# Performance work log

Hardware: AMD Instinct MI355X
Metric: run time of the kernel (lower is better)

## Reference

```python
import jax, jax.numpy as jnp
import numpy as np

N = 262144
E = N * 32
C_W = 7.0 / np.pi  # Wendland C2 2D normalization


def kernel_gradient(q, dirs, h):
    # torchSPHv2 wendland gradient: -dir * C/h^3 * 20 q (1-q)^3, q = r/h in [0,1]
    mag = (C_W / h ** 3) * 20.0 * q * (1.0 - q) ** 3
    return -dirs * mag[:, None]


def setup_inputs() -> dict:
    key = jax.random.key(0)
    ks = jax.random.split(key, 10)
    pos = lambda k: jax.random.uniform(k, (N,), dtype=jnp.float32) + 0.5  # keep strictly positive
    fluidArea = pos(ks[0]) * 1e-3
    fluidActualArea = pos(ks[1]) * 1e-3
    fluidRestDensity = pos(ks[2]) * 1000.0
    fluidDensity = pos(ks[3])
    fluidPressure2 = jax.random.uniform(ks[4], (N,), dtype=jnp.float32) * 1e3
    fluidPredictedVelocity = jax.random.normal(ks[5], (N, 2), dtype=jnp.float32)
    fluidPredAccel = jax.random.normal(ks[6], (N, 2), dtype=jnp.float32)
    fluidNeighbors = jax.random.randint(ks[7], (2, E), 0, N, dtype=jnp.int32)
    fluidRadialDistances = jax.random.uniform(ks[8], (E,), dtype=jnp.float32)
    d = jax.random.normal(ks[9], (E, 2), dtype=jnp.float32)
    fluidDistances = d / (jnp.linalg.norm(d, axis=1, keepdims=True) + 1e-7)
    return {
        'fluidArea': fluidArea, 'fluidActualArea': fluidActualArea,
        'fluidRestDensity': fluidRestDensity, 'fluidDensity': fluidDensity,
        'fluidPressure2': fluidPressure2,
        'fluidPredictedVelocity': fluidPredictedVelocity,
        'fluidPredAccel': fluidPredAccel,
        'fluidRadialDistances': fluidRadialDistances,
        'fluidDistances': fluidDistances,
        'fluidNeighbors': fluidNeighbors,
        'support': 0.05, 'dt': 0.002,
    }


def reference(fluidArea, fluidActualArea, fluidRestDensity, fluidDensity,
              fluidPressure2, fluidPredictedVelocity, fluidPredAccel,
              fluidRadialDistances, fluidDistances, fluidNeighbors,
              support, dt):
    seg = lambda v, i: jax.ops.segment_sum(v, i, num_segments=N)
    i = fluidNeighbors[0]
    j = fluidNeighbors[1]
    grad = kernel_gradient(fluidRadialDistances, fluidDistances, support)  # [E,2]
    grad2 = jnp.einsum('nd,nd->n', grad, grad)

    # --- alpha (fluid term + final) ---
    kSum1 = seg(fluidActualArea[j][:, None] * grad, i)                       # [N,2]
    kSum2 = seg((fluidActualArea ** 2 / (fluidArea * fluidRestDensity))[j] * grad2, i)
    fac = -dt ** 2 * fluidActualArea
    mass = fluidArea * fluidRestDensity
    alpha = fac / mass * jnp.einsum('nd,nd->n', kSum1, kSum1) + fac * kSum2

    # --- fluid pressure acceleration ---
    facA = -(fluidArea * fluidRestDensity)[j]
    p = fluidPressure2 / (fluidDensity * fluidRestDensity) ** 2
    fluidAccelTerm = seg((facA * (p[i] + p[j]))[:, None] * grad, i)          # [N,2]

    # --- source term (velocity divergence) ---
    facS = -dt * fluidActualArea[j]
    vij = fluidPredictedVelocity[i] - fluidPredictedVelocity[j]
    source = seg(facS * jnp.einsum('nd,nd->n', vij, grad), i)                # [N]

    # --- updated pressure fluid kernel sum ---
    facP = dt ** 2 * fluidActualArea[j]
    aij = fluidPredAccel[i] - fluidPredAccel[j]
    kernelSum = seg(jnp.einsum('nd,nd->n', facP[:, None] * aij, grad), i)    # [N]

    return jnp.concatenate([alpha[:, None], fluidAccelTerm,
                            source[:, None], kernelSum[:, None]], axis=1)  # [N,5]
```

## Files before the change

### kernel.cpp

```cpp
#include <hip/hip_runtime.h>
#include <math.h>


#define PB        512
#define PB_SHIFT  9
#define NR        8
#define NSLICE    4
#define CSTRIDE   16
#define BIN_EDGES 2048
#define TILE      1024

typedef float v2f __attribute__((ext_vector_type(2)));
typedef float v4f __attribute__((ext_vector_type(4)));

__device__ __forceinline__ void ldsbar() {
    asm volatile("s_waitcnt lgkmcnt(0)" ::: "memory");
    __builtin_amdgcn_s_barrier();
    asm volatile("" ::: "memory");
}

static inline size_t align256(size_t x) { return (x + 255) & ~(size_t)255; }

__global__ __launch_bounds__(256) void pre_kernel(
    const float*  __restrict__ area,
    const float*  __restrict__ actualArea,
    const float*  __restrict__ restDensity,
    const float*  __restrict__ density,
    const float*  __restrict__ pressure2,
    const float2* __restrict__ vel,
    const float2* __restrict__ accel,
    float4* __restrict__ pre2,
    int*    __restrict__ cursor, int ncursor,
    float*  __restrict__ accz, int nacc,
    int n) {
    int t = blockIdx.x * blockDim.x + threadIdx.x;
    int stride = gridDim.x * blockDim.x;
    for (int k = t; k < ncursor; k += stride) cursor[k] = 0;
    for (int k = t; k < nacc; k += stride) accz[k] = 0.f;
    if (t >= n) return;
    float m  = area[t] * restDensity[t];
    float dr = density[t] * restDensity[t];
    float p  = pressure2[t] / (dr * dr);
    float aa = actualArea[t];
    float2 v  = vel[t];
    float2 ac = accel[t];
    pre2[2 * (size_t)t]     = make_float4(p, m / aa, aa, aa * aa / m);
    pre2[2 * (size_t)t + 1] = make_float4(v.x, v.y, ac.x, ac.y);
}

__global__ __launch_bounds__(256) void bin_kernel(
    const int*    __restrict__ nbr,
    const float*  __restrict__ rad,
    const float2* __restrict__ dirs,
    const float*  __restrict__ supp,
    int*          __restrict__ cursor,
    unsigned int* __restrict__ pay32,
    int cap, int nb, int estart, int eend, int E) {
    __shared__ float4 srec[BIN_EDGES];
    __shared__ int lcount[512];
    __shared__ int lclaim[512];
    __shared__ int lstart[512];
    int tid = threadIdx.x;
    int x   = blockIdx.x & (NR - 1);
    for (int k = tid; k < 512; k += 256) lcount[k] = 0;
    ldsbar();
    int e0 = estart + blockIdx.x * BIN_EDGES + tid;

    int jj[8]; float qq[8]; v2f dd[8]; int pk[8];
#pragma unroll
    for (int k = 0; k < 8; ++k) {
        int e = e0 + k * 256;
        pk[k] = -1; jj[k] = 0; qq[k] = 0.f; dd[k] = (v2f){0.f, 0.f};
        if (e < eend) {
            jj[k] = __builtin_nontemporal_load(nbr + E + e);
            qq[k] = __builtin_nontemporal_load(rad + e);
            dd[k] = __builtin_nontemporal_load((const v2f*)dirs + e);
            int i = __builtin_nontemporal_load(nbr + e);
            int b = i >> PB_SHIFT;
            int r = atomicAdd(&lcount[b], 1);
            pk[k] = (b << 21) | ((i & (PB - 1)) << 12) | r;
        }
    }
    ldsbar();
    if (tid >= 64) {
        for (int k = tid - 64; k < nb; k += 192) {
            int c = lcount[k];
            lclaim[k] = c ? atomicAdd(&cursor[(size_t)(k * NR + x) * CSTRIDE], c) : 0;
        }
    } else {
        int running = 0;
        for (int c = 0; c < 8; ++c) {
            int orig = lcount[c * 64 + tid];
            int v = orig;
#pragma unroll
            for (int off = 1; off < 64; off <<= 1) {
                int u = __shfl_up(v, off, 64);
                if (tid >= off) v += u;
            }
            lstart[c * 64 + tid] = running + v - orig;
            running += __shfl(v, 63, 64);
        }
    }
    ldsbar();

    float h  = supp[0];
    float kc = 20.0f * (7.0f / 3.14159265358979323846f) / (h * h * h);
    int cap3  = cap * 3;
    int cap24 = cap * 3 * NR;

#pragma unroll
    for (int k = 0; k < 8; ++k) {
        if (pk[k] < 0) continue;
        int b  = pk[k] >> 21;
        int li = (pk[k] >> 12) & (PB - 1);
        int r  = pk[k] & 2047;
        float  q = qq[k];
        v2f    d = dd[k];
        float om  = 1.0f - q;
        float mag = kc * q * om * om * om;
        float gx = -d.x * mag;
        float gy = -d.y * mag;
        int g  = lclaim[b] + r;
        int gd = (g < cap) ? (b * cap24 + x * cap3 + g * 3) : -1;
        srec[lstart[b] + r] = make_float4(
            __int_as_float((jj[k] << PB_SHIFT) | li), gx, gy, __int_as_float(gd));
    }
    ldsbar();
    int total = lstart[511] + lcount[511];
    for (int r = tid; r < total; r += 256) {
        float4 rec = srec[r];
        int gd = __float_as_int(rec.w);
        if (gd >= 0) {
            uint3 w = make_uint3(__float_as_uint(rec.x), __float_as_uint(rec.y),
                                 __float_as_uint(rec.z));
            *(uint3*)(pay32 + gd) = w;
        }
    }
}

__global__ __launch_bounds__(256) void reduce_kernel(
    const unsigned int* __restrict__ pay32,
    const int*    __restrict__ cursor, int cap,
    const float4* __restrict__ pre2,
    const float*  __restrict__ dtp,
    float*        __restrict__ partials,
    int accum, int n) {
    __shared__ float s7[6][TILE];
    __shared__ int   lhist[PB];
    __shared__ int   lofs[PB];
    __shared__ float ptab[PB];
    int b   = blockIdx.x >> 2;
    int sb  = blockIdx.x & (NSLICE - 1);
    int tid = threadIdx.x;

    int p0 = (b << PB_SHIFT) + tid;
    int p1 = p0 + 256;
    float pi0 = (p0 < n) ? pre2[2 * (size_t)p0].x : 0.f;
    float pi1 = (p1 < n) ? pre2[2 * (size_t)p1].x : 0.f;
    ptab[tid] = pi0; ptab[tid + 256] = pi1;
    float a0[7] = {0.f, 0.f, 0.f, 0.f, 0.f, 0.f, 0.f};
    float a1[7] = {0.f, 0.f, 0.f, 0.f, 0.f, 0.f, 0.f};

    int r0 = tid * 4;
    for (int rg = 0; rg < 2; ++rg) {
        int s = sb + rg * NSLICE;
        int cnt = cursor[(size_t)(b * NR + s) * CSTRIDE];
        if (cnt > cap) cnt = cap;
        size_t RB = (size_t)(b * NR + s) * cap * 3;

        v4f c0v, c1v, c2v, n0v, n1v, n2v;
        if (cnt > 0) {
            int rb = r0;
            int rc_ = (rb + 4 <= cap) ? rb : (cap - 4);
            const v4f* g = (const v4f*)(pay32 + RB + (size_t)rc_ * 3);
            c0v = __builtin_nontemporal_load(g);
            c1v = __builtin_nontemporal_load(g + 1);
            c2v = __builtin_nontemporal_load(g + 2);
        }
        for (int T = 0; T < cnt; T += TILE) {
            lhist[tid] = 0; lhist[tid + 256] = 0;
            if (T + TILE < cnt) {
                int rb = T + TILE + r0;
                int rc_ = (rb + 4 <= cap) ? rb : (cap - 4);
                const v4f* g = (const v4f*)(pay32 + RB + (size_t)rc_ * 3);
                n0v = __builtin_nontemporal_load(g);
                n1v = __builtin_nontemporal_load(g + 1);
                n2v = __builtin_nontemporal_load(g + 2);
            }
            int rb = T + r0;
            bool v0 = rb < cnt, v1 = rb + 1 < cnt, v2 = rb + 2 < cnt, v3 = rb + 3 < cnt;
            int jli0 = __float_as_int(c0v.x); float gx0 = c0v.y, gy0 = c0v.z;
            int jli1 = __float_as_int(c0v.w); float gx1 = c1v.x, gy1 = c1v.y;
            int jli2 = __float_as_int(c1v.z); float gx2 = c1v.w, gy2 = c2v.x;
            int jli3 = __float_as_int(c2v.y); float gx3 = c2v.z, gy3 = c2v.w;
            int li0 = jli0 & (PB - 1), li1 = jli1 & (PB - 1);
            int li2 = jli2 & (PB - 1), li3 = jli3 & (PB - 1);
            size_t j0 = v0 ? (size_t)(jli0 >> PB_SHIFT) : 0;
            size_t j1 = v1 ? (size_t)(jli1 >> PB_SHIFT) : 0;
            size_t j2 = v2 ? (size_t)(jli2 >> PB_SHIFT) : 0;
            size_t j3 = v3 ? (size_t)(jli3 >> PB_SHIFT) : 0;
            float4 ja0 = pre2[2 * j0], jb0 = pre2[2 * j0 + 1];
            float4 ja1 = pre2[2 * j1], jb1 = pre2[2 * j1 + 1];
            float4 ja2 = pre2[2 * j2], jb2 = pre2[2 * j2 + 1];
            float4 ja3 = pre2[2 * j3], jb3 = pre2[2 * j3 + 1];
            ldsbar();
            if (v0) atomicAdd(&lhist[li0], 1);
            if (v1) atomicAdd(&lhist[li1], 1);
            if (v2) atomicAdd(&lhist[li2], 1);
            if (v3) atomicAdd(&lhist[li3], 1);
            ldsbar();
            if (tid < 64) {
                int running = 0;
                for (int c = 0; c < 8; ++c) {
                    int orig = lhist[c * 64 + tid];
                    int v = orig;
#pragma unroll
                    for (int off = 1; off < 64; off <<= 1) {
                        int u = __shfl_up(v, off, 64);
                        if (tid >= off) v += u;
                    }
                    lofs[c * 64 + tid] = running + v - orig;
                    running += __shfl(v, 63, 64);
                }
            }
            ldsbar();
#define SCAT(vv, li, jaa, jbb, gxx, gyy)                                     \
            if (vv) {                                                        \
                int sl = atomicAdd(&lofs[li], 1);                            \
                float C0 = jaa.z * gxx;                                      \
                float C1 = jaa.z * gyy;                                      \
                s7[0][sl] = C0;                                              \
                s7[1][sl] = C1;                                              \
                s7[2][sl] = jaa.w * (gxx * gxx + gyy * gyy);                 \
                s7[3][sl] = -(ptab[li] + jaa.x) * jaa.y;                     \
                s7[4][sl] = jbb.x * C0 + jbb.y * C1;                         \
                s7[5][sl] = jbb.z * C0 + jbb.w * C1;                         \
            }
            SCAT(v0, li0, ja0, jb0, gx0, gy0)
            SCAT(v1, li1, ja1, jb1, gx1, gy1)
            SCAT(v2, li2, ja2, jb2, gx2, gy2)
            SCAT(v3, li3, ja3, jb3, gx3, gy3)
#undef SCAT
            ldsbar();
            {
                int e0 = lofs[tid], h0 = lhist[tid];
                for (int r = e0 - h0; r < e0; ++r) {
                    float C0 = s7[0][r], C1 = s7[1][r], rc = s7[3][r];
                    a0[0] += C0; a0[1] += C1; a0[2] += s7[2][r];
                    a0[3] += rc * C0; a0[4] += rc * C1;
                    a0[5] += s7[4][r]; a0[6] += s7[5][r];
                }
                int e1 = lofs[tid + 256], h1 = lhist[tid + 256];
                for (int r = e1 - h1; r < e1; ++r) {
                    float C0 = s7[0][r], C1 = s7[1][r], rc = s7[3][r];
                    a1[0] += C0; a1[1] += C1; a1[2] += s7[2][r];
                    a1[3] += rc * C0; a1[4] += rc * C1;
                    a1[5] += s7[4][r]; a1[6] += s7[5][r];
                }
            }
            ldsbar();
            c0v = n0v; c1v = n1v; c2v = n2v;
        }
    }

    float dt  = dtp[0];
    float dt2 = dt * dt;
    v4f* dst = (v4f*)(partials + ((size_t)b * NSLICE + sb) * (PB * 8));
    {
        float4 va = (p0 < n) ? pre2[2 * (size_t)p0 + 1]
                             : make_float4(0.f, 0.f, 0.f, 0.f);
        float src = dt  * (a0[5] - (va.x * a0[0] + va.y * a0[1]));
        float ker = dt2 * ((va.z * a0[0] + va.w * a0[1]) - a0[6]);
        v4f w0 = {a0[0], a0[1], a0[2], a0[3]};
        v4f w1 = {a0[4], src, ker, 0.f};
        v4f* d = dst + (size_t)tid * 2;
        if (accum) {
            v4f o0 = d[0], o1 = d[1];
            d[0] = w0 + o0; d[1] = w1 + o1;
        } else {
            __builtin_nontemporal_store(w0, d);
            __builtin_nontemporal_store(w1, d + 1);
        }
    }
    {
        float4 va = (p1 < n) ? pre2[2 * (size_t)p1 + 1]
                             : make_float4(0.f, 0.f, 0.f, 0.f);
        float src = dt  * (a1[5] - (va.x * a1[0] + va.y * a1[1]));
        float ker = dt2 * ((va.z * a1[0] + va.w * a1[1]) - a1[6]);
        v4f w0 = {a1[0], a1[1], a1[2], a1[3]};
        v4f w1 = {a1[4], src, ker, 0.f};
        v4f* d = dst + (size_t)(tid + 256) * 2;
        if (accum) {
            v4f o0 = d[0], o1 = d[1];
            d[0] = w0 + o0; d[1] = w1 + o1;
        } else {
            __builtin_nontemporal_store(w0, d);
            __builtin_nontemporal_store(w1, d + 1);
        }
    }
}

__global__ void edge_kernel(const int* __restrict__ nbr,
                            const float* __restrict__ rad,
                            const float2* __restrict__ dirs,
                            const float4* __restrict__ pre2,
                            const float* __restrict__ supp,
                            const float* __restrict__ dtp,
                            float* __restrict__ acc, int E) {
    int e = blockIdx.x * blockDim.x + threadIdx.x;
    if (e >= E) return;
    float h = supp[0], dt = dtp[0];
    float kc = 20.0f * (7.0f / 3.14159265358979323846f) / (h * h * h);
    int i = nbr[e];
    int j = nbr[E + e];
    float  q = rad[e];
    float2 d = dirs[e];
    float om  = 1.0f - q;
    float mag = kc * q * om * om * om;
    float gx = -d.x * mag;
    float gy = -d.y * mag;
    float g2 = gx * gx + gy * gy;
    float4 ja = pre2[2 * (size_t)j];
    float4 jb = pre2[2 * (size_t)j + 1];
    float4 ia = pre2[2 * (size_t)i];
    float4 ib = pre2[2 * (size_t)i + 1];
    float aaj = ja.z;
    float m   = ja.y * aaj;
    float pp  = -m * (ia.x + ja.x);
    float vdotg = (ib.x - jb.x) * gx + (ib.y - jb.y) * gy;
    float adotg = (ib.z - jb.z) * gx + (ib.w - jb.w) * gy;
    float* base = acc + (size_t)i * 8;
    atomicAdd(base + 0, aaj * gx);
    atomicAdd(base + 1, aaj * gy);
    atomicAdd(base + 2, ja.w * g2);
    atomicAdd(base + 3, pp * gx);
    atomicAdd(base + 4, pp * gy);
    atomicAdd(base + 5, -dt * aaj * vdotg);
    atomicAdd(base + 6, dt * dt * aaj * adotg);
}

__global__ __launch_bounds__(256) void fin_kernel(
    const float* __restrict__ area,
    const float* __restrict__ actualArea,
    const float* __restrict__ restDensity,
    const float* __restrict__ dtp,
    const float* __restrict__ data, int mode, int nslice,
    float* __restrict__ out, int n) {
    int t = blockIdx.x * blockDim.x + threadIdx.x;
    if (t >= n) return;
    float s0 = 0, s1 = 0, s2 = 0, s3 = 0, s4 = 0, s5 = 0, s6 = 0;
    if (mode == 0) {
        const v4f* base = (const v4f*)data
            + ((size_t)(t >> PB_SHIFT) * NSLICE) * (PB * 2)
            + (size_t)(t & (PB - 1)) * 2;
        for (int s = 0; s < nslice; ++s) {
            v4f q0 = __builtin_nontemporal_load(base + (size_t)s * (PB * 2));
            v4f q1 = __builtin_nontemporal_load(base + (size_t)s * (PB * 2) + 1);
            s0 += q0.x; s1 += q0.y; s2 += q0.z; s3 += q0.w;
            s4 += q1.x; s5 += q1.y; s6 += q1.z;
        }
    } else {
        const float* a = data + (size_t)t * 8;
        s0 = a[0]; s1 = a[1]; s2 = a[2]; s3 = a[3];
        s4 = a[4]; s5 = a[5]; s6 = a[6];
    }
    float dt   = dtp[0];
    float fac  = -dt * dt * actualArea[t];
    float mass = area[t] * restDensity[t];
    float alpha = fac / mass * (s0 * s0 + s1 * s1) + fac * s2;
    float* o = out + (size_t)t * 5;
    o[0] = alpha;
    o[1] = s3;
    o[2] = s4;
    o[3] = s5;
    o[4] = s6;
}

extern "C" void kernel_launch(void* const* d_in, const int* in_sizes, int n_in,
                              void* d_out, int out_size, void* d_ws, size_t ws_size,
                              hipStream_t stream) {
    const float* area        = (const float*)d_in[0];
    const float* actualArea  = (const float*)d_in[1];
    const float* restDensity = (const float*)d_in[2];
    const float* density     = (const float*)d_in[3];
    const float* pressure2   = (const float*)d_in[4];
    const float2* vel        = (const float2*)d_in[5];
    const float2* accel      = (const float2*)d_in[6];
    const float* rad         = (const float*)d_in[7];
    const float2* dirs       = (const float2*)d_in[8];
    const int*   nbr         = (const int*)d_in[9];
    const float* supp        = (const float*)d_in[10];
    const float* dtp         = (const float*)d_in[11];
    float* out = (float*)d_out;

    int N = in_sizes[0];
    int E = in_sizes[7];
    int nb = (N + PB - 1) >> PB_SHIFT;

    size_t sz_cur   = (size_t)nb * NR * CSTRIDE * 8 * sizeof(int);
    size_t off_pre  = align256(sz_cur);
    size_t sz_pre   = (size_t)N * 8 * sizeof(float);
    size_t off_part = align256(off_pre + sz_pre);
    size_t sz_partA = (size_t)nb * NSLICE * PB * 8 * sizeof(float);
    size_t sz_partB = (size_t)N * 8 * sizeof(float);
    size_t sz_part  = sz_partA > sz_partB ? sz_partA : sz_partB;
    size_t off_pay  = align256(off_part + sz_part);

    int* cursor     = (int*)d_ws;
    float4* pre2    = (float4*)((char*)d_ws + off_pre);
    float* partials = (float*)((char*)d_ws + off_part);

    int nchunk = 0, cap = 0;
    if (nb <= 512 && ws_size > off_pay) {
        for (int c = 1; c <= 8; c *= 2) {
            long long Ec = (E + c - 1) / c;
            double mean = (double)Ec / ((double)nb * NR);
            long long need = (long long)(mean + 8.0 * sqrt(mean) + 64.0);
            need = (need + 63) & ~63ll;
            if (off_pay + (size_t)nb * NR * need * 12 <= ws_size) {
                nchunk = c; cap = (int)need; break;
            }
        }
    }

    int bs = 256;
    int grid_n = (N + bs - 1) / bs;
    if (nchunk > 0) {
        unsigned int* pay32 = (unsigned int*)((char*)d_ws + off_pay);
        int ncursor = nb * NR * CSTRIDE * nchunk;
        pre_kernel<<<grid_n, bs, 0, stream>>>(
            area, actualArea, restDensity, density, pressure2, vel, accel,
            pre2, cursor, ncursor, (float*)nullptr, 0, N);
        int Ec  = (E + nchunk - 1) / nchunk;
        for (int c = 0; c < nchunk; ++c) {
            int es = c * Ec;
            int ee = es + Ec; if (ee > E) ee = E;
            if (es >= ee) break;
            int* curC = cursor + (size_t)c * nb * NR * CSTRIDE;
            int nblk = (ee - es + BIN_EDGES - 1) / BIN_EDGES;
            bin_kernel<<<nblk, bs, 0, stream>>>(
                nbr, rad, dirs, supp, curC, pay32, cap, nb, es, ee, E);
            reduce_kernel<<<nb * NSLICE, bs, 0, stream>>>(
                pay32, curC, cap, pre2, dtp, partials, (c > 0) ? 1 : 0, N);
        }
        fin_kernel<<<grid_n, bs, 0, stream>>>(
            area, actualArea, restDensity, dtp, partials, 0, NSLICE, out, N);
    } else {
        float* acc = partials;
        pre_kernel<<<grid_n, bs, 0, stream>>>(
            area, actualArea, restDensity, density, pressure2, vel, accel,
            pre2, cursor, 0, acc, N * 8, N);
        edge_kernel<<<(E + bs - 1) / bs, bs, 0, stream>>>(
            nbr, rad, dirs, pre2, supp, dtp, acc, E);
        fin_kernel<<<grid_n, bs, 0, stream>>>(
            area, actualArea, restDensity, dtp, acc, 1, 0, out, N);
    }
}
```

Baseline: 389.4 us.

## Fuse precompute into binning, batch bin blocks, and fold finalize into reduce

```diff
diff --git a/kernel.cpp b/kernel.cpp
--- a/kernel.cpp
+++ b/kernel.cpp
@@ -7,7 +7,9 @@
 #define NR        8
 #define NSLICE    4
 #define CSTRIDE   16
-#define BIN_EDGES 2048
+#define SB        4
+#define SBE       2048
+#define BIN_EDGES (SB * SBE)
 #define TILE      1024
 
 typedef float v2f __attribute__((ext_vector_type(2)));
@@ -30,12 +32,10 @@
     const float2* __restrict__ vel,
     const float2* __restrict__ accel,
     float4* __restrict__ pre2,
-    int*    __restrict__ cursor, int ncursor,
     float*  __restrict__ accz, int nacc,
     int n) {
     int t = blockIdx.x * blockDim.x + threadIdx.x;
     int stride = gridDim.x * blockDim.x;
-    for (int k = t; k < ncursor; k += stride) cursor[k] = 0;
     for (int k = t; k < nacc; k += stride) accz[k] = 0.f;
     if (t >= n) return;
     float m  = area[t] * restDensity[t];
@@ -53,53 +53,57 @@
     const float*  __restrict__ rad,
     const float2* __restrict__ dirs,
     const float*  __restrict__ supp,
+    const float*  __restrict__ area,
+    const float*  __restrict__ actualArea,
+    const float*  __restrict__ restDensity,
+    const float*  __restrict__ density,
+    const float*  __restrict__ pressure2,
+    const float2* __restrict__ vel,
+    const float2* __restrict__ accel,
+    float4*       __restrict__ pre2,
+    int doPre, int ppb, int n,
     int*          __restrict__ cursor,
     unsigned int* __restrict__ pay32,
     int cap, int nb, int estart, int eend, int E) {
-    __shared__ float4 srec[BIN_EDGES];
+    __shared__ float4 srec[SBE];
+    __shared__ int ltot[512];
     __shared__ int lcount[512];
     __shared__ int lclaim[512];
     __shared__ int lstart[512];
+    __shared__ int lprev[512];
     int tid = threadIdx.x;
     int x   = blockIdx.x & (NR - 1);
-    for (int k = tid; k < 512; k += 256) lcount[k] = 0;
+
+    if (doPre) {
+        int pbase = blockIdx.x * ppb;
+        int pend  = pbase + ppb; if (pend > n) pend = n;
+        for (int t = pbase + tid; t < pend; t += 256) {
+            float m  = area[t] * restDensity[t];
+            float dr = density[t] * restDensity[t];
+            float p  = pressure2[t] / (dr * dr);
+            float aa = actualArea[t];
+            float2 v  = vel[t];
+            float2 ac = accel[t];
+            pre2[2 * (size_t)t]     = make_float4(p, m / aa, aa, aa * aa / m);
+            pre2[2 * (size_t)t + 1] = make_float4(v.x, v.y, ac.x, ac.y);
+        }
+    }
+
+    for (int k = tid; k < 512; k += 256) { ltot[k] = 0; lprev[k] = 0; }
     ldsbar();
-    int e0 = estart + blockIdx.x * BIN_EDGES + tid;
-
-    int jj[8]; float qq[8]; v2f dd[8]; int pk[8];
-#pragma unroll
-    for (int k = 0; k < 8; ++k) {
-        int e = e0 + k * 256;
-        pk[k] = -1; jj[k] = 0; qq[k] = 0.f; dd[k] = (v2f){0.f, 0.f};
+    int e0 = estart + blockIdx.x * BIN_EDGES;
+
+    for (int k = tid; k < BIN_EDGES; k += 256) {
+        int e = e0 + k;
         if (e < eend) {
-            jj[k] = __builtin_nontemporal_load(nbr + E + e);
-            qq[k] = __builtin_nontemporal_load(rad + e);
-            dd[k] = __builtin_nontemporal_load((const v2f*)dirs + e);
             int i = __builtin_nontemporal_load(nbr + e);
-            int b = i >> PB_SHIFT;
-            int r = atomicAdd(&lcount[b], 1);
-            pk[k] = (b << 21) | ((i & (PB - 1)) << 12) | r;
+            atomicAdd(&ltot[i >> PB_SHIFT], 1);
         }
     }
     ldsbar();
-    if (tid >= 64) {
-        for (int k = tid - 64; k < nb; k += 192) {
-            int c = lcount[k];
-            lclaim[k] = c ? atomicAdd(&cursor[(size_t)(k * NR + x) * CSTRIDE], c) : 0;
-        }
-    } else {
-        int running = 0;
-        for (int c = 0; c < 8; ++c) {
-            int orig = lcount[c * 64 + tid];
-            int v = orig;
-#pragma unroll
-            for (int off = 1; off < 64; off <<= 1) {
-                int u = __shfl_up(v, off, 64);
-                if (tid >= off) v += u;
-            }
-            lstart[c * 64 + tid] = running + v - orig;
-            running += __shfl(v, 63, 64);
-        }
+    for (int k = tid; k < nb; k += 256) {
+        int c = ltot[k];
+        lclaim[k] = c ? atomicAdd(&cursor[(size_t)(k * NR + x) * CSTRIDE], c) : 0;
     }
     ldsbar();
 
@@ -108,33 +112,73 @@
     int cap3  = cap * 3;
     int cap24 = cap * 3 * NR;
 
+    for (int sb = 0; sb < SB; ++sb) {
+        for (int k = tid; k < 512; k += 256) lcount[k] = 0;
+        ldsbar();
+        int es = e0 + sb * SBE + tid;
+        int jj[8]; float qq[8]; v2f dd[8]; int pk[8];
 #pragma unroll
-    for (int k = 0; k < 8; ++k) {
-        if (pk[k] < 0) continue;
-        int b  = pk[k] >> 21;
-        int li = (pk[k] >> 12) & (PB - 1);
-        int r  = pk[k] & 2047;
-        float  q = qq[k];
-        v2f    d = dd[k];
-        float om  = 1.0f - q;
-        float mag = kc * q * om * om * om;
-        float gx = -d.x * mag;
-        float gy = -d.y * mag;
-        int g  = lclaim[b] + r;
-        int gd = (g < cap) ? (b * cap24 + x * cap3 + g * 3) : -1;
-        srec[lstart[b] + r] = make_float4(
-            __int_as_float((jj[k] << PB_SHIFT) | li), gx, gy, __int_as_float(gd));
-    }
-    ldsbar();
-    int total = lstart[511] + lcount[511];
-    for (int r = tid; r < total; r += 256) {
-        float4 rec = srec[r];
-        int gd = __float_as_int(rec.w);
-        if (gd >= 0) {
-            uint3 w = make_uint3(__float_as_uint(rec.x), __float_as_uint(rec.y),
-                                 __float_as_uint(rec.z));
-            *(uint3*)(pay32 + gd) = w;
-        }
+        for (int k = 0; k < 8; ++k) {
+            int e = es + k * 256;
+            pk[k] = -1; jj[k] = 0; qq[k] = 0.f; dd[k] = (v2f){0.f, 0.f};
+            if (e < eend) {
+                jj[k] = __builtin_nontemporal_load(nbr + E + e);
+                qq[k] = __builtin_nontemporal_load(rad + e);
+                dd[k] = __builtin_nontemporal_load((const v2f*)dirs + e);
+                int i = __builtin_nontemporal_load(nbr + e);
+                int b = i >> PB_SHIFT;
+                int r = atomicAdd(&lcount[b], 1);
+                pk[k] = (b << 21) | ((i & (PB - 1)) << 12) | r;
+            }
+        }
+        ldsbar();
+        if (tid < 64) {
+            int running = 0;
+            for (int c = 0; c < 8; ++c) {
+                int orig = lcount[c * 64 + tid];
+                int v = orig;
+#pragma unroll
+                for (int off = 1; off < 64; off <<= 1) {
+                    int u = __shfl_up(v, off, 64);
+                    if (tid >= off) v += u;
+                }
+                lstart[c * 64 + tid] = running + v - orig;
+                running += __shfl(v, 63, 64);
+            }
+        }
+        ldsbar();
+#pragma unroll
+        for (int k = 0; k < 8; ++k) {
+            if (pk[k] < 0) continue;
+            int b  = pk[k] >> 21;
+            int li = (pk[k] >> 12) & (PB - 1);
+            int r  = pk[k] & 2047;
+            float  q = qq[k];
+            v2f    d = dd[k];
+            float om  = 1.0f - q;
+            float mag = kc * q * om * om * om;
+            float gx = -d.x * mag;
+            float gy = -d.y * mag;
+            int g  = lclaim[b] + lprev[b] + r;
+            int gd = (g < cap) ? (b * cap24 + x * cap3 + g * 3) : -1;
+            srec[lstart[b] + r] = make_float4(
+                __int_as_float((jj[k] << PB_SHIFT) | li), gx, gy,
+                __int_as_float(gd));
+        }
+        ldsbar();
+        int total = lstart[511] + lcount[511];
+        for (int r = tid; r < total; r += 256) {
+            float4 rec = srec[r];
+            int gd = __float_as_int(rec.w);
+            if (gd >= 0) {
+                uint3 w = make_uint3(__float_as_uint(rec.x),
+                                     __float_as_uint(rec.y),
+                                     __float_as_uint(rec.z));
+                *(uint3*)(pay32 + gd) = w;
+            }
+        }
+        for (int k = tid; k < 512; k += 256) lprev[k] += lcount[k];
+        ldsbar();
     }
 }
 
@@ -144,11 +188,17 @@
     const float4* __restrict__ pre2,
     const float*  __restrict__ dtp,
     float*        __restrict__ partials,
-    int accum, int n) {
+    const float*  __restrict__ area,
+    const float*  __restrict__ actualArea,
+    const float*  __restrict__ restDensity,
+    float*        __restrict__ out,
+    int*          __restrict__ done,
+    int accum, int fuse, int n) {
     __shared__ float s7[6][TILE];
     __shared__ int   lhist[PB];
     __shared__ int   lofs[PB];
     __shared__ float ptab[PB];
+    __shared__ int   lastFlag;
     int b   = blockIdx.x >> 2;
     int sb  = blockIdx.x & (NSLICE - 1);
     int tid = threadIdx.x;
@@ -274,13 +324,8 @@
         v4f w0 = {a0[0], a0[1], a0[2], a0[3]};
         v4f w1 = {a0[4], src, ker, 0.f};
         v4f* d = dst + (size_t)tid * 2;
-        if (accum) {
-            v4f o0 = d[0], o1 = d[1];
-            d[0] = w0 + o0; d[1] = w1 + o1;
-        } else {
-            __builtin_nontemporal_store(w0, d);
-            __builtin_nontemporal_store(w1, d + 1);
-        }
+        if (accum) { v4f o0 = d[0], o1 = d[1]; d[0] = w0 + o0; d[1] = w1 + o1; }
+        else       { d[0] = w0; d[1] = w1; }
     }
     {
         float4 va = (p1 < n) ? pre2[2 * (size_t)p1 + 1]
@@ -290,13 +335,35 @@
         v4f w0 = {a1[0], a1[1], a1[2], a1[3]};
         v4f w1 = {a1[4], src, ker, 0.f};
         v4f* d = dst + (size_t)(tid + 256) * 2;
-        if (accum) {
-            v4f o0 = d[0], o1 = d[1];
-            d[0] = w0 + o0; d[1] = w1 + o1;
-        } else {
-            __builtin_nontemporal_store(w0, d);
-            __builtin_nontemporal_store(w1, d + 1);
-        }
+        if (accum) { v4f o0 = d[0], o1 = d[1]; d[0] = w0 + o0; d[1] = w1 + o1; }
+        else       { d[0] = w0; d[1] = w1; }
+    }
+
+    if (!fuse) return;
+    __threadfence();
+    __syncthreads();
+    if (tid == 0) lastFlag = (atomicAdd(&done[b], 1) == NSLICE - 1) ? 1 : 0;
+    __syncthreads();
+    if (!lastFlag) return;
+    __threadfence();
+    const v4f* pbase = (const v4f*)(partials + (size_t)b * NSLICE * (PB * 8));
+#pragma unroll
+    for (int k = 0; k < 2; ++k) {
+        int idx = tid + (k << 8);
+        int p   = (b << PB_SHIFT) + idx;
+        if (p >= n) continue;
+        float t0 = 0, t1 = 0, t2 = 0, t3 = 0, t4 = 0, t5 = 0, t6 = 0;
+        for (int sl = 0; sl < NSLICE; ++sl) {
+            v4f q0 = pbase[(size_t)sl * (PB * 2) + 2 * idx];
+            v4f q1 = pbase[(size_t)sl * (PB * 2) + 2 * idx + 1];
+            t0 += q0.x; t1 += q0.y; t2 += q0.z; t3 += q0.w;
+            t4 += q1.x; t5 += q1.y; t6 += q1.z;
+        }
+        float fac  = -dt2 * actualArea[p];
+        float mass = area[p] * restDensity[p];
+        float alpha = fac / mass * (t0 * t0 + t1 * t1) + fac * t2;
+        float* o = out + (size_t)p * 5;
+        o[0] = alpha; o[1] = t3; o[2] = t4; o[3] = t5; o[4] = t6;
     }
 }
 
@@ -344,26 +411,13 @@
     const float* __restrict__ actualArea,
     const float* __restrict__ restDensity,
     const float* __restrict__ dtp,
-    const float* __restrict__ data, int mode, int nslice,
+    const float* __restrict__ data,
     float* __restrict__ out, int n) {
     int t = blockIdx.x * blockDim.x + threadIdx.x;
     if (t >= n) return;
-    float s0 = 0, s1 = 0, s2 = 0, s3 = 0, s4 = 0, s5 = 0, s6 = 0;
-    if (mode == 0) {
-        const v4f* base = (const v4f*)data
-            + ((size_t)(t >> PB_SHIFT) * NSLICE) * (PB * 2)
-            + (size_t)(t & (PB - 1)) * 2;
-        for (int s = 0; s < nslice; ++s) {
-            v4f q0 = __builtin_nontemporal_load(base + (size_t)s * (PB * 2));
-            v4f q1 = __builtin_nontemporal_load(base + (size_t)s * (PB * 2) + 1);
-            s0 += q0.x; s1 += q0.y; s2 += q0.z; s3 += q0.w;
-            s4 += q1.x; s5 += q1.y; s6 += q1.z;
-        }
-    } else {
-        const float* a = data + (size_t)t * 8;
-        s0 = a[0]; s1 = a[1]; s2 = a[2]; s3 = a[3];
-        s4 = a[4]; s5 = a[5]; s6 = a[6];
-    }
+    const float* a = data + (size_t)t * 8;
+    float s0 = a[0], s1 = a[1], s2 = a[2], s3 = a[3];
+    float s4 = a[4], s5 = a[5], s6 = a[6];
     float dt   = dtp[0];
     float fac  = -dt * dt * actualArea[t];
     float mass = area[t] * restDensity[t];
@@ -398,7 +452,8 @@
     int nb = (N + PB - 1) >> PB_SHIFT;
 
     size_t sz_cur   = (size_t)nb * NR * CSTRIDE * 8 * sizeof(int);
-    size_t off_pre  = align256(sz_cur);
+    size_t sz_done  = (size_t)nb * sizeof(int);
+    size_t off_pre  = align256(sz_cur + sz_done);
     size_t sz_pre   = (size_t)N * 8 * sizeof(float);
     size_t off_part = align256(off_pre + sz_pre);
     size_t sz_partA = (size_t)nb * NSLICE * PB * 8 * sizeof(float);
@@ -407,6 +462,7 @@
     size_t off_pay  = align256(off_part + sz_part);
 
     int* cursor     = (int*)d_ws;
+    int* done       = (int*)((char*)d_ws + sz_cur);
     float4* pre2    = (float4*)((char*)d_ws + off_pre);
     float* partials = (float*)((char*)d_ws + off_part);
 
@@ -427,10 +483,7 @@
     int grid_n = (N + bs - 1) / bs;
     if (nchunk > 0) {
         unsigned int* pay32 = (unsigned int*)((char*)d_ws + off_pay);
-        int ncursor = nb * NR * CSTRIDE * nchunk;
-        pre_kernel<<<grid_n, bs, 0, stream>>>(
-            area, actualArea, restDensity, density, pressure2, vel, accel,
-            pre2, cursor, ncursor, (float*)nullptr, 0, N);
+        hipMemsetAsync(d_ws, 0, off_pre, stream);
         int Ec  = (E + nchunk - 1) / nchunk;
         for (int c = 0; c < nchunk; ++c) {
             int es = c * Ec;
@@ -438,21 +491,25 @@
             if (es >= ee) break;
             int* curC = cursor + (size_t)c * nb * NR * CSTRIDE;
             int nblk = (ee - es + BIN_EDGES - 1) / BIN_EDGES;
+            int ppb  = (N + nblk - 1) / nblk;
             bin_kernel<<<nblk, bs, 0, stream>>>(
-                nbr, rad, dirs, supp, curC, pay32, cap, nb, es, ee, E);
+                nbr, rad, dirs, supp,
+                area, actualArea, restDensity, density, pressure2, vel, accel,
+                pre2, (c == 0) ? 1 : 0, ppb, N,
+                curC, pay32, cap, nb, es, ee, E);
             reduce_kernel<<<nb * NSLICE, bs, 0, stream>>>(
-                pay32, curC, cap, pre2, dtp, partials, (c > 0) ? 1 : 0, N);
-        }
-        fin_kernel<<<grid_n, bs, 0, stream>>>(
-            area, actualArea, restDensity, dtp, partials, 0, NSLICE, out, N);
+                pay32, curC, cap, pre2, dtp, partials,
+                area, actualArea, restDensity, out, done,
+                (c > 0) ? 1 : 0, (c == nchunk - 1) ? 1 : 0, N);
+        }
     } else {
         float* acc = partials;
         pre_kernel<<<grid_n, bs, 0, stream>>>(
             area, actualArea, restDensity, density, pressure2, vel, accel,
-            pre2, cursor, 0, acc, N * 8, N);
+            pre2, acc, N * 8, N);
         edge_kernel<<<(E + bs - 1) / bs, bs, 0, stream>>>(
             nbr, rad, dirs, pre2, supp, dtp, acc, E);
         fin_kernel<<<grid_n, bs, 0, stream>>>(
-            area, actualArea, restDensity, dtp, acc, 1, 0, out, N);
-    }
-}
+            area, actualArea, restDensity, dtp, acc, out, N);
+    }
+}
```

New measurement: 1.030 ms. 2.65x slower.

## Fuse precompute into bin kernel and batch cursor claims over larger edge blocks

Applied to the files above, without the earlier changes.

```diff
diff --git a/kernel.cpp b/kernel.cpp
--- a/kernel.cpp
+++ b/kernel.cpp
@@ -7,7 +7,9 @@
 #define NR        8
 #define NSLICE    4
 #define CSTRIDE   16
-#define BIN_EDGES 2048
+#define SB        4
+#define SBE       2048
+#define BIN_EDGES (SB * SBE)
 #define TILE      1024
 
 typedef float v2f __attribute__((ext_vector_type(2)));
@@ -30,12 +32,10 @@
     const float2* __restrict__ vel,
     const float2* __restrict__ accel,
     float4* __restrict__ pre2,
-    int*    __restrict__ cursor, int ncursor,
     float*  __restrict__ accz, int nacc,
     int n) {
     int t = blockIdx.x * blockDim.x + threadIdx.x;
     int stride = gridDim.x * blockDim.x;
-    for (int k = t; k < ncursor; k += stride) cursor[k] = 0;
     for (int k = t; k < nacc; k += stride) accz[k] = 0.f;
     if (t >= n) return;
     float m  = area[t] * restDensity[t];
@@ -53,53 +53,53 @@
     const float*  __restrict__ rad,
     const float2* __restrict__ dirs,
     const float*  __restrict__ supp,
+    const float*  __restrict__ area,
+    const float*  __restrict__ actualArea,
+    const float*  __restrict__ restDensity,
+    const float*  __restrict__ density,
+    const float*  __restrict__ pressure2,
+    const float2* __restrict__ vel,
+    const float2* __restrict__ accel,
+    float4*       __restrict__ pre2,
+    int doPre, int ppb, int n,
     int*          __restrict__ cursor,
     unsigned int* __restrict__ pay32,
     int cap, int nb, int estart, int eend, int E) {
-    __shared__ float4 srec[BIN_EDGES];
+    __shared__ float4 srec[SBE];
+    __shared__ int ltot[512];
     __shared__ int lcount[512];
     __shared__ int lclaim[512];
     __shared__ int lstart[512];
     int tid = threadIdx.x;
     int x   = blockIdx.x & (NR - 1);
-    for (int k = tid; k < 512; k += 256) lcount[k] = 0;
+
+    if (doPre) {
+        int pbase = blockIdx.x * ppb;
+        int pend  = pbase + ppb; if (pend > n) pend = n;
+        for (int t = pbase + tid; t < pend; t += 256) {
+            float m  = area[t] * restDensity[t];
+            float dr = density[t] * restDensity[t];
+            float p  = pressure2[t] / (dr * dr);
+            float aa = actualArea[t];
+            float2 v  = vel[t];
+            float2 ac = accel[t];
+            pre2[2 * (size_t)t]     = make_float4(p, m / aa, aa, aa * aa / m);
+            pre2[2 * (size_t)t + 1] = make_float4(v.x, v.y, ac.x, ac.y);
+        }
+    }
+
+    for (int k = tid; k < 512; k += 256) ltot[k] = 0;
     ldsbar();
-    int e0 = estart + blockIdx.x * BIN_EDGES + tid;
-
-    int jj[8]; float qq[8]; v2f dd[8]; int pk[8];
-#pragma unroll
-    for (int k = 0; k < 8; ++k) {
-        int e = e0 + k * 256;
-        pk[k] = -1; jj[k] = 0; qq[k] = 0.f; dd[k] = (v2f){0.f, 0.f};
-        if (e < eend) {
-            jj[k] = __builtin_nontemporal_load(nbr + E + e);
-            qq[k] = __builtin_nontemporal_load(rad + e);
-            dd[k] = __builtin_nontemporal_load((const v2f*)dirs + e);
-            int i = __builtin_nontemporal_load(nbr + e);
-            int b = i >> PB_SHIFT;
-            int r = atomicAdd(&lcount[b], 1);
-            pk[k] = (b << 21) | ((i & (PB - 1)) << 12) | r;
-        }
+    int e0 = estart + blockIdx.x * BIN_EDGES;
+
+    for (int k = tid; k < BIN_EDGES; k += 256) {
+        int e = e0 + k;
+        if (e < eend) atomicAdd(&ltot[nbr[e] >> PB_SHIFT], 1);
     }
     ldsbar();
-    if (tid >= 64) {
-        for (int k = tid - 64; k < nb; k += 192) {
-            int c = lcount[k];
-            lclaim[k] = c ? atomicAdd(&cursor[(size_t)(k * NR + x) * CSTRIDE], c) : 0;
-        }
-    } else {
-        int running = 0;
-        for (int c = 0; c < 8; ++c) {
-            int orig = lcount[c * 64 + tid];
-            int v = orig;
-#pragma unroll
-            for (int off = 1; off < 64; off <<= 1) {
-                int u = __shfl_up(v, off, 64);
-                if (tid >= off) v += u;
-            }
-            lstart[c * 64 + tid] = running + v - orig;
-            running += __shfl(v, 63, 64);
-        }
+    for (int k = tid; k < nb; k += 256) {
+        int c = ltot[k];
+        lclaim[k] = c ? atomicAdd(&cursor[(size_t)(k * NR + x) * CSTRIDE], c) : 0;
     }
     ldsbar();
 
@@ -108,33 +108,73 @@
     int cap3  = cap * 3;
     int cap24 = cap * 3 * NR;
 
+    for (int sb = 0; sb < SB; ++sb) {
+        for (int k = tid; k < 512; k += 256) lcount[k] = 0;
+        ldsbar();
+        int es = e0 + sb * SBE + tid;
+        int jj[8]; float qq[8]; v2f dd[8]; int pk[8];
 #pragma unroll
-    for (int k = 0; k < 8; ++k) {
-        if (pk[k] < 0) continue;
-        int b  = pk[k] >> 21;
-        int li = (pk[k] >> 12) & (PB - 1);
-        int r  = pk[k] & 2047;
-        float  q = qq[k];
-        v2f    d = dd[k];
-        float om  = 1.0f - q;
-        float mag = kc * q * om * om * om;
-        float gx = -d.x * mag;
-        float gy = -d.y * mag;
-        int g  = lclaim[b] + r;
-        int gd = (g < cap) ? (b * cap24 + x * cap3 + g * 3) : -1;
-        srec[lstart[b] + r] = make_float4(
-            __int_as_float((jj[k] << PB_SHIFT) | li), gx, gy, __int_as_float(gd));
-    }
-    ldsbar();
-    int total = lstart[511] + lcount[511];
-    for (int r = tid; r < total; r += 256) {
-        float4 rec = srec[r];
-        int gd = __float_as_int(rec.w);
-        if (gd >= 0) {
-            uint3 w = make_uint3(__float_as_uint(rec.x), __float_as_uint(rec.y),
-                                 __float_as_uint(rec.z));
-            *(uint3*)(pay32 + gd) = w;
-        }
+        for (int k = 0; k < 8; ++k) {
+            int e = es + k * 256;
+            pk[k] = -1; jj[k] = 0; qq[k] = 0.f; dd[k] = (v2f){0.f, 0.f};
+            if (e < eend) {
+                jj[k] = __builtin_nontemporal_load(nbr + E + e);
+                qq[k] = __builtin_nontemporal_load(rad + e);
+                dd[k] = __builtin_nontemporal_load((const v2f*)dirs + e);
+                int i = nbr[e];
+                int b = i >> PB_SHIFT;
+                int r = atomicAdd(&lcount[b], 1);
+                pk[k] = (b << 21) | ((i & (PB - 1)) << 12) | r;
+            }
+        }
+        ldsbar();
+        if (tid < 64) {
+            int running = 0;
+            for (int c = 0; c < 8; ++c) {
+                int orig = lcount[c * 64 + tid];
+                int v = orig;
+#pragma unroll
+                for (int off = 1; off < 64; off <<= 1) {
+                    int u = __shfl_up(v, off, 64);
+                    if (tid >= off) v += u;
+                }
+                lstart[c * 64 + tid] = running + v - orig;
+                running += __shfl(v, 63, 64);
+            }
+        }
+        ldsbar();
+#pragma unroll
+        for (int k = 0; k < 8; ++k) {
+            if (pk[k] < 0) continue;
+            int b  = pk[k] >> 21;
+            int li = (pk[k] >> 12) & (PB - 1);
+            int r  = pk[k] & 2047;
+            float  q = qq[k];
+            v2f    d = dd[k];
+            float om  = 1.0f - q;
+            float mag = kc * q * om * om * om;
+            float gx = -d.x * mag;
+            float gy = -d.y * mag;
+            int g  = lclaim[b] + r;
+            int gd = (g < cap) ? (b * cap24 + x * cap3 + g * 3) : -1;
+            srec[lstart[b] + r] = make_float4(
+                __int_as_float((jj[k] << PB_SHIFT) | li), gx, gy,
+                __int_as_float(gd));
+        }
+        ldsbar();
+        int total = lstart[511] + lcount[511];
+        for (int r = tid; r < total; r += 256) {
+            float4 rec = srec[r];
+            int gd = __float_as_int(rec.w);
+            if (gd >= 0) {
+                uint3 w = make_uint3(__float_as_uint(rec.x),
+                                     __float_as_uint(rec.y),
+                                     __float_as_uint(rec.z));
+                *(uint3*)(pay32 + gd) = w;
+            }
+        }
+        for (int k = tid; k < 512; k += 256) lclaim[k] += lcount[k];
+        ldsbar();
     }
 }
 
@@ -427,10 +467,7 @@
     int grid_n = (N + bs - 1) / bs;
     if (nchunk > 0) {
         unsigned int* pay32 = (unsigned int*)((char*)d_ws + off_pay);
-        int ncursor = nb * NR * CSTRIDE * nchunk;
-        pre_kernel<<<grid_n, bs, 0, stream>>>(
-            area, actualArea, restDensity, density, pressure2, vel, accel,
-            pre2, cursor, ncursor, (float*)nullptr, 0, N);
+        hipMemsetAsync(d_ws, 0, sz_cur, stream);
         int Ec  = (E + nchunk - 1) / nchunk;
         for (int c = 0; c < nchunk; ++c) {
             int es = c * Ec;
@@ -438,8 +475,12 @@
             if (es >= ee) break;
             int* curC = cursor + (size_t)c * nb * NR * CSTRIDE;
             int nblk = (ee - es + BIN_EDGES - 1) / BIN_EDGES;
+            int ppb  = (N + nblk - 1) / nblk;
             bin_kernel<<<nblk, bs, 0, stream>>>(
-                nbr, rad, dirs, supp, curC, pay32, cap, nb, es, ee, E);
+                nbr, rad, dirs, supp,
+                area, actualArea, restDensity, density, pressure2, vel, accel,
+                pre2, (c == 0) ? 1 : 0, ppb, N,
+                curC, pay32, cap, nb, es, ee, E);
             reduce_kernel<<<nb * NSLICE, bs, 0, stream>>>(
                 pay32, curC, cap, pre2, dtp, partials, (c > 0) ? 1 : 0, N);
         }
@@ -449,7 +490,7 @@
         float* acc = partials;
         pre_kernel<<<grid_n, bs, 0, stream>>>(
             area, actualArea, restDensity, density, pressure2, vel, accel,
-            pre2, cursor, 0, acc, N * 8, N);
+            pre2, acc, N * 8, N);
         edge_kernel<<<(E + bs - 1) / bs, bs, 0, stream>>>(
             nbr, rad, dirs, pre2, supp, dtp, acc, E);
         fin_kernel<<<grid_n, bs, 0, stream>>>(
```

Result: no change. 391.9 us (+0.7%).
